# Kernel tuning notes

Hardware: AMD Instinct MI355X
Metric: run time of the kernel (lower is better)

## Reference

```python
import jax, jax.numpy as jnp
import numpy as np

H, D, K = 8, 512, 64
EPS = 1e-12


def _l2norm(x):
    # F.normalize(p=2, dim=-1): x / max(||x||_2, eps)
    n = jnp.sqrt(jnp.sum(x * x, axis=-1, keepdims=True))
    return x / jnp.maximum(n, EPS)


def setup_inputs() -> dict:
    key = jax.random.key(0)
    ks = jax.random.split(key, 8)
    S, B = 1024, 16
    scale = 1.0 / np.sqrt(D)
    return {
        "query": jax.random.normal(ks[0], (S, B, D), dtype=jnp.float32),
        "key": jax.random.normal(ks[1], (S, B, D), dtype=jnp.float32),
        "value": jax.random.normal(ks[2], (S, B, D), dtype=jnp.float32),
        # stacked per-head projection weights, torch Linear convention [out,in]
        "WQ": jax.random.uniform(ks[3], (H, K, D), jnp.float32, -scale, scale),
        "WK": jax.random.uniform(ks[4], (H, K, D), jnp.float32, -scale, scale),
        "WV": jax.random.uniform(ks[5], (H, K, D), jnp.float32, -scale, scale),
        "Wout": jax.random.uniform(ks[6], (D, H * K), jnp.float32,
                                   -1.0 / np.sqrt(H * K), 1.0 / np.sqrt(H * K)),
    }


def reference(query, key, value, WQ, WK, WV, Wout):
    temp = K ** 0.5
    # project all heads at once: [S,B,D] x [H,K,D] -> [B,H,S,K]
    wq = _l2norm(jnp.einsum("sbd,hkd->bhsk", query, WQ))
    wk = _l2norm(jnp.einsum("sbd,hkd->bhsk", key, WK))
    wv = _l2norm(jnp.einsum("sbd,hkd->bhsk", value, WV))
    # cosine-similarity attention scores [B,H,Sq,Sk]
    scores = jnp.einsum("bhsk,bhtk->bhst", wq, wk) / temp
    aff = jax.nn.softmax(scores, axis=-1)
    out = jnp.einsum("bhst,bhtk->bhsk", aff, wv)  # [B,H,S,K]
    # concat heads -> [S,B,H*K] (matches torch per-head concat on last dim)
    Sq, B = query.shape[0], query.shape[1]
    concat = out.transpose(2, 0, 1, 3).reshape(Sq, B, H * K)
    return concat @ Wout.T  # [S,B,D]
```

## Files before the change

kernel.cpp:

```cpp
#include <hip/hip_runtime.h>
#include <cstdint>
#include <cstddef>

typedef unsigned int u32;
typedef unsigned short u16;
typedef __attribute__((ext_vector_type(8))) short short8;
typedef __attribute__((ext_vector_type(4))) float f32x4;

#define S_LEN 1024
#define BATCH 16
#define NHEAD 8
#define DMODEL 512
#define KHD 64
#define NROW (S_LEN * BATCH)

__device__ __forceinline__ u16 f2bf(float f) {
    u32 u = __float_as_uint(f);
    return (u16)((u + 0x7fffu + ((u >> 16) & 1u)) >> 16);
}

__device__ __forceinline__ void gl_lds16(const void* g, void* l) {
    __builtin_amdgcn_global_load_lds(
        (const __attribute__((address_space(1))) void*)(uintptr_t)g,
        (__attribute__((address_space(3))) void*)(uintptr_t)l, 16, 0, 0);
}

__global__ __launch_bounds__(256) void wcvt_kernel(
    const float* __restrict__ WQ, const float* __restrict__ WK,
    const float* __restrict__ WV, const float* __restrict__ Wo,
    u16* __restrict__ dst)
{
    const int m = blockIdx.y;
    const float* __restrict__ src = (m == 0) ? WQ : (m == 1) ? WK : (m == 2) ? WV : Wo;
    const int idx = (blockIdx.x * 256 + threadIdx.x) * 4;
    const float4 v = *(const float4*)(src + idx);
    u16 r[4];
    r[0] = f2bf(v.x); r[1] = f2bf(v.y); r[2] = f2bf(v.z); r[3] = f2bf(v.w);
    *(uint2*)(dst + (size_t)m * DMODEL * DMODEL + idx) = *(uint2*)r;
}

template<int M>
__global__ __launch_bounds__(256) void gemm_kernel(
    const float* __restrict__ A0,
    const float* __restrict__ A1,
    const u16* __restrict__ Abf,
    const u16* __restrict__ Wb,
    u16* __restrict__ outN,
    float* __restrict__ outP)
{
    __shared__ __align__(16) u16 Alds[128 * 64];
    __shared__ __align__(16) u16 Blds[128 * 64];

    const int tid  = threadIdx.x;
    const int wave = tid >> 6;
    const int lane = tid & 63;
    const int m16  = lane & 15;
    const int quad = lane >> 4;
    const int wm   = wave >> 1;
    const int wn   = wave & 1;
    const int n0   = blockIdx.y * 128;
    const int row0 = blockIdx.x * 128;
    const int z    = (M == 1) ? blockIdx.z : 0;
    const int bb   = (M == 2) ? blockIdx.z : 0;

    const float* __restrict__ A32 =
        (M == 1) ? (z ? A1 : A0) : (M == 2) ? (A0 + (size_t)bb * DMODEL) : nullptr;
    const size_t astr = (M == 2) ? (size_t)BATCH * DMODEL : (size_t)DMODEL;
    const u16* __restrict__ B = Wb + ((M == 1) ? (size_t)z * DMODEL * DMODEL : 0);

    f32x4 acc[4][4] = {};

    const int brow   = lane >> 3;
    const int bchunk = (lane & 7) ^ brow;

    for (int kt = 0; kt < DMODEL; kt += 64) {
        __syncthreads();
        {
            u16* la = &Alds[(wave * 32) * 64];
            u16* lb = &Blds[(wave * 32) * 64];
            const u16* bp = B + (size_t)(n0 + wave * 32 + brow) * DMODEL + kt + bchunk * 8;
            if (M == 0) {
                const int colc = kt + bchunk * 8;
                const int hh   = colc >> 6;
                const int kk   = colc & 63;
#pragma unroll
                for (int j = 0; j < 4; j++) {
                    const int i  = row0 + wave * 32 + brow + j * 8;
                    const int ss = i >> 4, bx = i & 15;
                    gl_lds16(Abf + (((size_t)(bx * NHEAD + hh) * S_LEN + ss) * KHD + kk),
                             la + j * 8 * 64);
                    gl_lds16(bp + (size_t)j * 8 * DMODEL, lb + j * 8 * 64);
                }
            } else {
                const int acf = lane & 7;
                float4 av[8];
#pragma unroll
                for (int j = 0; j < 8; j++) {
                    const int rl = wave * 32 + (j & 3) * 8 + brow;
                    const int cf = (j >> 2) * 8 + acf;
                    av[j] = *(const float4*)(A32 + (size_t)(row0 + rl) * astr + kt + cf * 4);
                }
#pragma unroll
                for (int j = 0; j < 4; j++)
                    gl_lds16(bp + (size_t)j * 8 * DMODEL, lb + j * 8 * 64);
#pragma unroll
                for (int j = 0; j < 8; j++) {
                    const int rl = wave * 32 + (j & 3) * 8 + brow;
                    const int cf = (j >> 2) * 8 + acf;
                    u32 lo, hi;
                    asm("v_cvt_pk_bf16_f32 %0, %1, %2" : "=v"(lo) : "v"(av[j].x), "v"(av[j].y));
                    asm("v_cvt_pk_bf16_f32 %0, %1, %2" : "=v"(hi) : "v"(av[j].z), "v"(av[j].w));
                    uint2 pk; pk.x = lo; pk.y = hi;
                    *(uint2*)&Alds[rl * 64 + (((cf >> 1) ^ (rl & 7)) << 3) + ((cf & 1) << 2)] = pk;
                }
            }
        }
        __syncthreads();

#pragma unroll
        for (int half = 0; half < 2; half++) {
            short8 af[4], bfr[4];
#pragma unroll
            for (int mt = 0; mt < 4; mt++)
                af[mt] = *(const short8*)&Alds[(wm * 64 + mt * 16 + m16) * 64 +
                                               (((half << 2) + quad) ^ (m16 & 7)) * 8];
#pragma unroll
            for (int nt = 0; nt < 4; nt++)
                bfr[nt] = *(const short8*)&Blds[(wn * 64 + nt * 16 + m16) * 64 +
                                                (((half << 2) + quad) ^ (m16 & 7)) * 8];
#pragma unroll
            for (int mt = 0; mt < 4; mt++)
#pragma unroll
                for (int nt = 0; nt < 4; nt++)
                    acc[mt][nt] = __builtin_amdgcn_mfma_f32_16x16x32_bf16(af[mt], bfr[nt], acc[mt][nt], 0, 0, 0);
        }
    }

    if (M == 1) {
        const int h = (n0 >> 6) + wn;
        u16* outZ = outN + (size_t)z * BATCH * NHEAD * S_LEN * KHD;
#pragma unroll
        for (int mt = 0; mt < 4; mt++) {
#pragma unroll
            for (int r = 0; r < 4; r++) {
                float ss = 0.0f;
#pragma unroll
                for (int nt = 0; nt < 4; nt++) ss += acc[mt][nt][r] * acc[mt][nt][r];
                ss += __shfl_xor(ss, 1);
                ss += __shfl_xor(ss, 2);
                ss += __shfl_xor(ss, 4);
                ss += __shfl_xor(ss, 8);
                const float sc = 1.0f / fmaxf(sqrtf(ss), 1e-12f);
                const int i = row0 + wm * 64 + mt * 16 + quad * 4 + r;
                const int s = i >> 4, b = i & 15;
                u16* op = outZ + (((size_t)b * NHEAD + h) * S_LEN + s) * KHD;
#pragma unroll
                for (int nt = 0; nt < 4; nt++)
                    op[nt * 16 + m16] = f2bf(acc[mt][nt][r] * sc);
            }
        }
    } else if (M == 2) {
        const int h = (n0 >> 6) + wn;
#pragma unroll
        for (int mt = 0; mt < 4; mt++) {
            float scl[4];
#pragma unroll
            for (int r = 0; r < 4; r++) {
                float ss = 0.0f;
#pragma unroll
                for (int nt = 0; nt < 4; nt++) ss += acc[mt][nt][r] * acc[mt][nt][r];
                ss += __shfl_xor(ss, 1);
                ss += __shfl_xor(ss, 2);
                ss += __shfl_xor(ss, 4);
                ss += __shfl_xor(ss, 8);
                scl[r] = 1.0f / fmaxf(sqrtf(ss), 1e-12f);
            }
            const int sbase = row0 + wm * 64 + mt * 16 + quad * 4;
#pragma unroll
            for (int nt = 0; nt < 4; nt++) {
                const int vcol = nt * 16 + m16;
                uint2 pk;
                pk.x = (u32)f2bf(acc[mt][nt][0] * scl[0]) |
                       ((u32)f2bf(acc[mt][nt][1] * scl[1]) << 16);
                pk.y = (u32)f2bf(acc[mt][nt][2] * scl[2]) |
                       ((u32)f2bf(acc[mt][nt][3] * scl[3]) << 16);
                u16* dp = outN + (((size_t)bb * NHEAD + h) * KHD + vcol) * S_LEN + sbase;
                *(uint2*)dp = pk;
            }
        }
    } else {
#pragma unroll
        for (int mt = 0; mt < 4; mt++) {
#pragma unroll
            for (int r = 0; r < 4; r++) {
                const int i = row0 + wm * 64 + mt * 16 + quad * 4 + r;
                float* op = outP + (size_t)i * DMODEL + n0 + wn * 64;
#pragma unroll
                for (int nt = 0; nt < 4; nt++)
                    op[nt * 16 + m16] = acc[mt][nt][r];
            }
        }
    }
}

__global__ __launch_bounds__(256, 2) void attn_kernel(
    const u16* __restrict__ wq, const u16* __restrict__ wk, const u16* __restrict__ wvT,
    u16* __restrict__ Xout)
{
    __shared__ __align__(16) u16 Klds[2][64 * 64];
    __shared__ __align__(16) u16 Vlds[2][64 * 64];
    __shared__ __align__(16) u16 Plds[4][4][16 * 32];

    const int tid  = threadIdx.x;
    const int wave = tid >> 6;
    const int lane = tid & 63;
    const int m16  = lane & 15;
    const int quad = lane >> 4;
    const int bh   = blockIdx.x;
    const int qt   = blockIdx.y;

    const u16* Qb = wq  + (size_t)bh * S_LEN * KHD;
    const u16* Kb = wk  + (size_t)bh * S_LEN * KHD;
    const u16* Vb = wvT + (size_t)bh * KHD * S_LEN;

    const int qr0 = qt * 256 + wave * 64;
    short8 qf[4][2];
#pragma unroll
    for (int qb = 0; qb < 4; qb++) {
        qf[qb][0] = *(const short8*)(Qb + (size_t)(qr0 + qb * 16 + m16) * KHD + quad * 8);
        qf[qb][1] = *(const short8*)(Qb + (size_t)(qr0 + qb * 16 + m16) * KHD + 32 + quad * 8);
    }

    short8 ones;
#pragma unroll
    for (int j = 0; j < 8; j++) ones[j] = (short)0x3F80;

    f32x4 o[4][4] = {};
    f32x4 ls[4]   = {};
    const float C1 = 0.125f, C2 = 0.0078125f;

    const int srow   = lane >> 3;
    const int schunk = (lane & 7) ^ srow;
    const int r0     = wave * 8 + srow;
    const int pswz   = (m16 >> 1) & 3;

    gl_lds16(Kb + (size_t)r0 * KHD + schunk * 8,               &Klds[0][(wave * 8) * 64]);
    gl_lds16(Kb + (size_t)(r0 + 32) * KHD + schunk * 8,        &Klds[0][(wave * 8 + 32) * 64]);
    gl_lds16(Vb + (size_t)r0 * S_LEN + schunk * 8,             &Vlds[0][(wave * 8) * 64]);
    gl_lds16(Vb + (size_t)(r0 + 32) * S_LEN + schunk * 8,      &Vlds[0][(wave * 8 + 32) * 64]);
    __syncthreads();

    for (int it = 0; it < S_LEN / 64; it++) {
        const int cur = it & 1;

        if (it + 1 < S_LEN / 64) {
            const int nxt = cur ^ 1;
            const int kt0 = (it + 1) * 64;
            gl_lds16(Kb + (size_t)(kt0 + r0) * KHD + schunk * 8,        &Klds[nxt][(wave * 8) * 64]);
            gl_lds16(Kb + (size_t)(kt0 + r0 + 32) * KHD + schunk * 8,   &Klds[nxt][(wave * 8 + 32) * 64]);
            gl_lds16(Vb + (size_t)r0 * S_LEN + kt0 + schunk * 8,        &Vlds[nxt][(wave * 8) * 64]);
            gl_lds16(Vb + (size_t)(r0 + 32) * S_LEN + kt0 + schunk * 8, &Vlds[nxt][(wave * 8 + 32) * 64]);
        }

#pragma unroll
        for (int cc = 0; cc < 2; cc++) {
#pragma unroll
            for (int mm = 0; mm < 2; mm++) {
                const int mt = cc * 2 + mm;
                const short8 kf0 = *(const short8*)&Klds[cur][(mt * 16 + m16) * 64 + (quad ^ (m16 & 7)) * 8];
                const short8 kf1 = *(const short8*)&Klds[cur][(mt * 16 + m16) * 64 + ((4 + quad) ^ (m16 & 7)) * 8];
#pragma unroll
                for (int qb = 0; qb < 4; qb++) {
                    f32x4 s = {};
                    s = __builtin_amdgcn_mfma_f32_16x16x32_bf16(kf0, qf[qb][0], s, 0, 0, 0);
                    s = __builtin_amdgcn_mfma_f32_16x16x32_bf16(kf1, qf[qb][1], s, 0, 0, 0);
                    u32 up[4];
#pragma unroll
                    for (int r = 0; r < 4; r++) {
                        const float y = s[r];
                        const float p = fmaf(fmaf(C2, y, C1), y, 1.0f);
                        up[r] = __float_as_uint(p);
                    }
                    uint2 pk;
                    pk.x = __builtin_amdgcn_perm(up[1], up[0], 0x07060302u);
                    pk.y = __builtin_amdgcn_perm(up[3], up[2], 0x07060302u);
                    *(uint2*)((char*)&Plds[wave][qb][0] + m16 * 64 +
                              ((((mm << 1) + (quad >> 1)) ^ pswz) << 4) + ((quad & 1) << 3)) = pk;
                }
            }

            short8 vfr[4];
#pragma unroll
            for (int vt = 0; vt < 4; vt++)
                vfr[vt] = *(const short8*)&Vlds[cur][(vt * 16 + m16) * 64 +
                                                     (((cc << 2) + quad) ^ (m16 & 7)) * 8];
            __builtin_amdgcn_s_setprio(1);
#pragma unroll
            for (int qb = 0; qb < 4; qb++) {
                const short8 pb = *(const short8*)((const char*)&Plds[wave][qb][0] + m16 * 64 +
                                                   ((quad ^ pswz) << 4));
                ls[qb] = __builtin_amdgcn_mfma_f32_16x16x32_bf16(ones, pb, ls[qb], 0, 0, 0);
#pragma unroll
                for (int vt = 0; vt < 4; vt++)
                    o[qb][vt] = __builtin_amdgcn_mfma_f32_16x16x32_bf16(vfr[vt], pb, o[qb][vt], 0, 0, 0);
            }
            __builtin_amdgcn_s_setprio(0);
        }

        __syncthreads();
    }

    u16* outB = Xout + (size_t)bh * S_LEN * KHD;
#pragma unroll
    for (int qb = 0; qb < 4; qb++) {
        const float inv = 1.0f / ls[qb][0];
        const int qrow = qr0 + qb * 16 + m16;
        u16* cp = outB + (size_t)qrow * KHD;
#pragma unroll
        for (int vt = 0; vt < 4; vt++) {
            uint2 pk;
            pk.x = (u32)f2bf(o[qb][vt][0] * inv) | ((u32)f2bf(o[qb][vt][1] * inv) << 16);
            pk.y = (u32)f2bf(o[qb][vt][2] * inv) | ((u32)f2bf(o[qb][vt][3] * inv) << 16);
            *(uint2*)(cp + vt * 16 + quad * 4) = pk;
        }
    }
}

extern "C" void kernel_launch(void* const* d_in, const int* in_sizes, int n_in,
                              void* d_out, int out_size, void* d_ws, size_t ws_size,
                              hipStream_t stream) {
    const float* q    = (const float*)d_in[0];
    const float* k    = (const float*)d_in[1];
    const float* v    = (const float*)d_in[2];
    const float* WQ   = (const float*)d_in[3];
    const float* WK   = (const float*)d_in[4];
    const float* WV   = (const float*)d_in[5];
    const float* Wout = (const float*)d_in[6];
    float* out = (float*)d_out;

    const size_t per = (size_t)BATCH * NHEAD * S_LEN * KHD;
    u16* wsQKV = (u16*)d_ws;
    u16* wsW   = wsQKV + 3 * per;

    wcvt_kernel<<<dim3(256, 4), 256, 0, stream>>>(WQ, WK, WV, Wout, wsW);

    gemm_kernel<1><<<dim3(NROW / 128, DMODEL / 128, 2), 256, 0, stream>>>(
        q, k, nullptr, wsW, wsQKV, nullptr);

    gemm_kernel<2><<<dim3(S_LEN / 128, DMODEL / 128, BATCH), 256, 0, stream>>>(
        v, nullptr, nullptr, wsW + (size_t)2 * DMODEL * DMODEL, wsQKV + 2 * per, nullptr);

    attn_kernel<<<dim3(BATCH * NHEAD, S_LEN / 256), 256, 0, stream>>>(
        wsQKV, wsQKV + per, wsQKV + 2 * per, wsQKV);

    gemm_kernel<0><<<dim3(NROW / 128, DMODEL / 128, 1), 256, 0, stream>>>(
        nullptr, nullptr, wsQKV, wsW + (size_t)3 * DMODEL * DMODEL, nullptr, out);
}
```

Measured before the change: 239.6 us.

## Double-buffer GEMM LDS tiles to overlap next-tile loads with MFMA compute

The GEMM main loop now uses two LDS buffers for A and B. Loads for tile k+1 (async global-to-LDS for B and bf16 A, register loads for fp32 A) are issued before computing tile k, and the fp32 A tile is converted and written to LDS after compute. This replaces the two barriers per iteration with one and aims to hide global-memory latency behind the matrix math. In exchange it doubles LDS use to 64 KB per block and holds the prefetched A registers live across compute. The launch bounds now request 2 blocks per CU, which may cap registers.

```diff
diff --git a/kernel.cpp b/kernel.cpp
--- a/kernel.cpp
+++ b/kernel.cpp
@@ -40,7 +40,7 @@
 }
 
 template<int M>
-__global__ __launch_bounds__(256) void gemm_kernel(
+__global__ __launch_bounds__(256, 2) void gemm_kernel(
     const float* __restrict__ A0,
     const float* __restrict__ A1,
     const u16* __restrict__ Abf,
@@ -48,8 +48,8 @@
     u16* __restrict__ outN,
     float* __restrict__ outP)
 {
-    __shared__ __align__(16) u16 Alds[128 * 64];
-    __shared__ __align__(16) u16 Blds[128 * 64];
+    __shared__ __align__(16) u16 Alds[2][128 * 64];
+    __shared__ __align__(16) u16 Blds[2][128 * 64];
 
     const int tid  = threadIdx.x;
     const int wave = tid >> 6;
@@ -72,68 +72,85 @@
 
     const int brow   = lane >> 3;
     const int bchunk = (lane & 7) ^ brow;
-
-    for (int kt = 0; kt < DMODEL; kt += 64) {
-        __syncthreads();
-        {
-            u16* la = &Alds[(wave * 32) * 64];
-            u16* lb = &Blds[(wave * 32) * 64];
-            const u16* bp = B + (size_t)(n0 + wave * 32 + brow) * DMODEL + kt + bchunk * 8;
-            if (M == 0) {
-                const int colc = kt + bchunk * 8;
-                const int hh   = colc >> 6;
-                const int kk   = colc & 63;
-#pragma unroll
-                for (int j = 0; j < 4; j++) {
-                    const int i  = row0 + wave * 32 + brow + j * 8;
-                    const int ss = i >> 4, bx = i & 15;
-                    gl_lds16(Abf + (((size_t)(bx * NHEAD + hh) * S_LEN + ss) * KHD + kk),
-                             la + j * 8 * 64);
-                    gl_lds16(bp + (size_t)j * 8 * DMODEL, lb + j * 8 * 64);
-                }
-            } else {
-                const int acf = lane & 7;
-                float4 av[8];
-#pragma unroll
-                for (int j = 0; j < 8; j++) {
-                    const int rl = wave * 32 + (j & 3) * 8 + brow;
-                    const int cf = (j >> 2) * 8 + acf;
-                    av[j] = *(const float4*)(A32 + (size_t)(row0 + rl) * astr + kt + cf * 4);
-                }
-#pragma unroll
-                for (int j = 0; j < 4; j++)
-                    gl_lds16(bp + (size_t)j * 8 * DMODEL, lb + j * 8 * 64);
-#pragma unroll
-                for (int j = 0; j < 8; j++) {
-                    const int rl = wave * 32 + (j & 3) * 8 + brow;
-                    const int cf = (j >> 2) * 8 + acf;
-                    u32 lo, hi;
-                    asm("v_cvt_pk_bf16_f32 %0, %1, %2" : "=v"(lo) : "v"(av[j].x), "v"(av[j].y));
-                    asm("v_cvt_pk_bf16_f32 %0, %1, %2" : "=v"(hi) : "v"(av[j].z), "v"(av[j].w));
-                    uint2 pk; pk.x = lo; pk.y = hi;
-                    *(uint2*)&Alds[rl * 64 + (((cf >> 1) ^ (rl & 7)) << 3) + ((cf & 1) << 2)] = pk;
-                }
-            }
-        }
-        __syncthreads();
-
+    const int acf    = lane & 7;
+
+    float4 av[8];
+
+    auto stage_B = [&](int kt, int b) {
+        const u16* bp = B + (size_t)(n0 + wave * 32 + brow) * DMODEL + kt + bchunk * 8;
+        u16* lb = &Blds[b][(wave * 32) * 64];
+#pragma unroll
+        for (int j = 0; j < 4; j++)
+            gl_lds16(bp + (size_t)j * 8 * DMODEL, lb + j * 8 * 64);
+    };
+    auto stage_A0 = [&](int kt, int b) {
+        u16* la = &Alds[b][(wave * 32) * 64];
+        const int colc = kt + bchunk * 8;
+        const int hh   = colc >> 6;
+        const int kk   = colc & 63;
+#pragma unroll
+        for (int j = 0; j < 4; j++) {
+            const int i  = row0 + wave * 32 + brow + j * 8;
+            const int ss = i >> 4, bx = i & 15;
+            gl_lds16(Abf + (((size_t)(bx * NHEAD + hh) * S_LEN + ss) * KHD + kk),
+                     la + j * 8 * 64);
+        }
+    };
+    auto load_A = [&](int kt) {
+#pragma unroll
+        for (int j = 0; j < 8; j++) {
+            const int rl = wave * 32 + (j & 3) * 8 + brow;
+            const int cf = (j >> 2) * 8 + acf;
+            av[j] = *(const float4*)(A32 + (size_t)(row0 + rl) * astr + kt + cf * 4);
+        }
+    };
+    auto write_A = [&](int b) {
+#pragma unroll
+        for (int j = 0; j < 8; j++) {
+            const int rl = wave * 32 + (j & 3) * 8 + brow;
+            const int cf = (j >> 2) * 8 + acf;
+            u32 lo, hi;
+            asm("v_cvt_pk_bf16_f32 %0, %1, %2" : "=v"(lo) : "v"(av[j].x), "v"(av[j].y));
+            asm("v_cvt_pk_bf16_f32 %0, %1, %2" : "=v"(hi) : "v"(av[j].z), "v"(av[j].w));
+            uint2 pk; pk.x = lo; pk.y = hi;
+            *(uint2*)&Alds[b][rl * 64 + (((cf >> 1) ^ (rl & 7)) << 3) + ((cf & 1) << 2)] = pk;
+        }
+    };
+    auto compute = [&](int b) {
 #pragma unroll
         for (int half = 0; half < 2; half++) {
             short8 af[4], bfr[4];
 #pragma unroll
             for (int mt = 0; mt < 4; mt++)
-                af[mt] = *(const short8*)&Alds[(wm * 64 + mt * 16 + m16) * 64 +
-                                               (((half << 2) + quad) ^ (m16 & 7)) * 8];
+                af[mt] = *(const short8*)&Alds[b][(wm * 64 + mt * 16 + m16) * 64 +
+                                                  (((half << 2) + quad) ^ (m16 & 7)) * 8];
 #pragma unroll
             for (int nt = 0; nt < 4; nt++)
-                bfr[nt] = *(const short8*)&Blds[(wn * 64 + nt * 16 + m16) * 64 +
-                                                (((half << 2) + quad) ^ (m16 & 7)) * 8];
+                bfr[nt] = *(const short8*)&Blds[b][(wn * 64 + nt * 16 + m16) * 64 +
+                                                   (((half << 2) + quad) ^ (m16 & 7)) * 8];
 #pragma unroll
             for (int mt = 0; mt < 4; mt++)
 #pragma unroll
                 for (int nt = 0; nt < 4; nt++)
                     acc[mt][nt] = __builtin_amdgcn_mfma_f32_16x16x32_bf16(af[mt], bfr[nt], acc[mt][nt], 0, 0, 0);
         }
+    };
+
+    if (M == 0) { stage_A0(0, 0); stage_B(0, 0); }
+    else        { load_A(0); stage_B(0, 0); write_A(0); }
+    __syncthreads();
+
+#pragma unroll 2
+    for (int it = 0; it < 8; it++) {
+        const int cur = it & 1;
+        const int nxt = cur ^ 1;
+        if (it < 7) {
+            if (M == 0) { stage_A0((it + 1) * 64, nxt); stage_B((it + 1) * 64, nxt); }
+            else        { load_A((it + 1) * 64);        stage_B((it + 1) * 64, nxt); }
+        }
+        compute(cur);
+        if (M != 0 && it < 7) write_A(nxt);
+        __syncthreads();
     }
 
     if (M == 1) {
```

New measurement: 241.7 us. No clear change (+0.9%).

## Split output projection into double-buffered 512-thread GEMM kernel

Applied to the files above, without the earlier changes.

The output-projection GEMM (M==0 path) moves out of the templated gemm_kernel into a dedicated gemm_out_kernel. It uses 8 waves per block, each holding a 32x64 accumulator tile, and double-buffered LDS with async global-to-LDS loads. Explicit vmcnt waits and barriers let the next K-tile load overlap the current tile's MFMA work. This aims to hide memory latency and raise occupancy, at the cost of twice the LDS per block and hand-tuned wait counts that must match the issued loads.

```diff
diff --git a/kernel.cpp b/kernel.cpp
--- a/kernel.cpp
+++ b/kernel.cpp
@@ -43,10 +43,8 @@
 __global__ __launch_bounds__(256) void gemm_kernel(
     const float* __restrict__ A0,
     const float* __restrict__ A1,
-    const u16* __restrict__ Abf,
     const u16* __restrict__ Wb,
-    u16* __restrict__ outN,
-    float* __restrict__ outP)
+    u16* __restrict__ outN)
 {
     __shared__ __align__(16) u16 Alds[128 * 64];
     __shared__ __align__(16) u16 Blds[128 * 64];
@@ -64,7 +62,7 @@
     const int bb   = (M == 2) ? blockIdx.z : 0;
 
     const float* __restrict__ A32 =
-        (M == 1) ? (z ? A1 : A0) : (M == 2) ? (A0 + (size_t)bb * DMODEL) : nullptr;
+        (M == 1) ? (z ? A1 : A0) : (A0 + (size_t)bb * DMODEL);
     const size_t astr = (M == 2) ? (size_t)BATCH * DMODEL : (size_t)DMODEL;
     const u16* __restrict__ B = Wb + ((M == 1) ? (size_t)z * DMODEL * DMODEL : 0);
 
@@ -72,47 +70,32 @@
 
     const int brow   = lane >> 3;
     const int bchunk = (lane & 7) ^ brow;
+    const int acf    = lane & 7;
 
     for (int kt = 0; kt < DMODEL; kt += 64) {
         __syncthreads();
         {
-            u16* la = &Alds[(wave * 32) * 64];
+            const u16* bp = B + (size_t)(n0 + wave * 32 + brow) * DMODEL + kt + bchunk * 8;
             u16* lb = &Blds[(wave * 32) * 64];
-            const u16* bp = B + (size_t)(n0 + wave * 32 + brow) * DMODEL + kt + bchunk * 8;
-            if (M == 0) {
-                const int colc = kt + bchunk * 8;
-                const int hh   = colc >> 6;
-                const int kk   = colc & 63;
-#pragma unroll
-                for (int j = 0; j < 4; j++) {
-                    const int i  = row0 + wave * 32 + brow + j * 8;
-                    const int ss = i >> 4, bx = i & 15;
-                    gl_lds16(Abf + (((size_t)(bx * NHEAD + hh) * S_LEN + ss) * KHD + kk),
-                             la + j * 8 * 64);
-                    gl_lds16(bp + (size_t)j * 8 * DMODEL, lb + j * 8 * 64);
-                }
-            } else {
-                const int acf = lane & 7;
-                float4 av[8];
-#pragma unroll
-                for (int j = 0; j < 8; j++) {
-                    const int rl = wave * 32 + (j & 3) * 8 + brow;
-                    const int cf = (j >> 2) * 8 + acf;
-                    av[j] = *(const float4*)(A32 + (size_t)(row0 + rl) * astr + kt + cf * 4);
-                }
-#pragma unroll
-                for (int j = 0; j < 4; j++)
-                    gl_lds16(bp + (size_t)j * 8 * DMODEL, lb + j * 8 * 64);
-#pragma unroll
-                for (int j = 0; j < 8; j++) {
-                    const int rl = wave * 32 + (j & 3) * 8 + brow;
-                    const int cf = (j >> 2) * 8 + acf;
-                    u32 lo, hi;
-                    asm("v_cvt_pk_bf16_f32 %0, %1, %2" : "=v"(lo) : "v"(av[j].x), "v"(av[j].y));
-                    asm("v_cvt_pk_bf16_f32 %0, %1, %2" : "=v"(hi) : "v"(av[j].z), "v"(av[j].w));
-                    uint2 pk; pk.x = lo; pk.y = hi;
-                    *(uint2*)&Alds[rl * 64 + (((cf >> 1) ^ (rl & 7)) << 3) + ((cf & 1) << 2)] = pk;
-                }
+            float4 av[8];
+#pragma unroll
+            for (int j = 0; j < 8; j++) {
+                const int rl = wave * 32 + (j & 3) * 8 + brow;
+                const int cf = (j >> 2) * 8 + acf;
+                av[j] = *(const float4*)(A32 + (size_t)(row0 + rl) * astr + kt + cf * 4);
+            }
+#pragma unroll
+            for (int j = 0; j < 4; j++)
+                gl_lds16(bp + (size_t)j * 8 * DMODEL, lb + j * 8 * 64);
+#pragma unroll
+            for (int j = 0; j < 8; j++) {
+                const int rl = wave * 32 + (j & 3) * 8 + brow;
+                const int cf = (j >> 2) * 8 + acf;
+                u32 lo, hi;
+                asm("v_cvt_pk_bf16_f32 %0, %1, %2" : "=v"(lo) : "v"(av[j].x), "v"(av[j].y));
+                asm("v_cvt_pk_bf16_f32 %0, %1, %2" : "=v"(hi) : "v"(av[j].z), "v"(av[j].w));
+                uint2 pk; pk.x = lo; pk.y = hi;
+                *(uint2*)&Alds[rl * 64 + (((cf >> 1) ^ (rl & 7)) << 3) + ((cf & 1) << 2)] = pk;
             }
         }
         __syncthreads();
@@ -153,13 +136,15 @@
                 const float sc = 1.0f / fmaxf(sqrtf(ss), 1e-12f);
                 const int i = row0 + wm * 64 + mt * 16 + quad * 4 + r;
                 const int s = i >> 4, b = i & 15;
-                u16* op = outZ + (((size_t)b * NHEAD + h) * S_LEN + s) * KHD;
+                u16* op = outN + (size_t)z * BATCH * NHEAD * S_LEN * KHD +
+                          (((size_t)b * NHEAD + h) * S_LEN + s) * KHD;
+                (void)outZ;
 #pragma unroll
                 for (int nt = 0; nt < 4; nt++)
                     op[nt * 16 + m16] = f2bf(acc[mt][nt][r] * sc);
             }
         }
-    } else if (M == 2) {
+    } else {
         const int h = (n0 >> 6) + wn;
 #pragma unroll
         for (int mt = 0; mt < 4; mt++) {
@@ -188,17 +173,101 @@
                 *(uint2*)dp = pk;
             }
         }
-    } else {
-#pragma unroll
-        for (int mt = 0; mt < 4; mt++) {
-#pragma unroll
-            for (int r = 0; r < 4; r++) {
-                const int i = row0 + wm * 64 + mt * 16 + quad * 4 + r;
-                float* op = outP + (size_t)i * DMODEL + n0 + wn * 64;
+    }
+}
+
+__global__ __launch_bounds__(512, 2) void gemm_out_kernel(
+    const u16* __restrict__ Abf,
+    const u16* __restrict__ Wb,
+    float* __restrict__ outP)
+{
+    __shared__ __align__(16) u16 Alds[2][128 * 64];
+    __shared__ __align__(16) u16 Blds[2][128 * 64];
+
+    const int tid  = threadIdx.x;
+    const int wave = tid >> 6;
+    const int lane = tid & 63;
+    const int m16  = lane & 15;
+    const int quad = lane >> 4;
+    const int wm   = wave >> 1;
+    const int wn   = wave & 1;
+    const int n0   = blockIdx.y * 128;
+    const int row0 = blockIdx.x * 128;
+
+    const int brow   = lane >> 3;
+    const int bchunk = (lane & 7) ^ brow;
+
+    f32x4 acc[2][4] = {};
+
+    auto stage = [&](int kt, int b) {
+        const int colc = kt + bchunk * 8;
+        const int hh   = colc >> 6;
+        const int kk   = colc & 63;
+        u16* la = &Alds[b][(wave * 16) * 64];
+#pragma unroll
+        for (int j = 0; j < 2; j++) {
+            const int i  = row0 + wave * 16 + j * 8 + brow;
+            const int ss = i >> 4, bx = i & 15;
+            gl_lds16(Abf + (((size_t)(bx * NHEAD + hh) * S_LEN + ss) * KHD + kk),
+                     la + j * 8 * 64);
+        }
+        const u16* bp = Wb + (size_t)(n0 + wave * 16 + brow) * DMODEL + kt + bchunk * 8;
+        u16* lb = &Blds[b][(wave * 16) * 64];
+#pragma unroll
+        for (int j = 0; j < 2; j++)
+            gl_lds16(bp + (size_t)j * 8 * DMODEL, lb + j * 8 * 64);
+    };
+    auto compute = [&](int b) {
+#pragma unroll
+        for (int half = 0; half < 2; half++) {
+            short8 af[2], bfr[4];
+#pragma unroll
+            for (int mt = 0; mt < 2; mt++)
+                af[mt] = *(const short8*)&Alds[b][(wm * 32 + mt * 16 + m16) * 64 +
+                                                  (((half << 2) + quad) ^ (m16 & 7)) * 8];
+#pragma unroll
+            for (int nt = 0; nt < 4; nt++)
+                bfr[nt] = *(const short8*)&Blds[b][(wn * 64 + nt * 16 + m16) * 64 +
+                                                   (((half << 2) + quad) ^ (m16 & 7)) * 8];
+#pragma unroll
+            for (int mt = 0; mt < 2; mt++)
 #pragma unroll
                 for (int nt = 0; nt < 4; nt++)
-                    op[nt * 16 + m16] = acc[mt][nt][r];
-            }
+                    acc[mt][nt] = __builtin_amdgcn_mfma_f32_16x16x32_bf16(af[mt], bfr[nt], acc[mt][nt], 0, 0, 0);
+        }
+    };
+
+    stage(0, 0);
+    stage(64, 1);
+    asm volatile("s_waitcnt vmcnt(4)" ::: "memory");
+    __builtin_amdgcn_s_barrier();
+    __builtin_amdgcn_sched_barrier(0);
+
+#pragma unroll
+    for (int t = 0; t < 8; t++) {
+        compute(t & 1);
+        if (t < 6) {
+            __builtin_amdgcn_s_barrier();
+            __builtin_amdgcn_sched_barrier(0);
+            stage((t + 2) * 64, t & 1);
+        }
+        if (t < 7) {
+            if (t < 6) asm volatile("s_waitcnt vmcnt(4)" ::: "memory");
+            else       asm volatile("s_waitcnt vmcnt(0)" ::: "memory");
+            __builtin_amdgcn_s_barrier();
+            __builtin_amdgcn_sched_barrier(0);
+        }
+    }
+
+#pragma unroll
+    for (int mt = 0; mt < 2; mt++) {
+#pragma unroll
+        for (int r = 0; r < 4; r++) {
+            const int i = row0 + wm * 32 + mt * 16 + quad * 4 + r;
+            float* op = outP + (size_t)i * DMODEL + n0 + wn * 64;
+#pragma unroll
+            for (int nt = 0; nt < 4; nt++)
+                op[nt * 16 + m16] = acc[mt][nt][r];
         }
     }
 }
@@ -345,14 +414,14 @@
     wcvt_kernel<<<dim3(256, 4), 256, 0, stream>>>(WQ, WK, WV, Wout, wsW);
 
     gemm_kernel<1><<<dim3(NROW / 128, DMODEL / 128, 2), 256, 0, stream>>>(
-        q, k, nullptr, wsW, wsQKV, nullptr);
+        q, k, wsW, wsQKV);
 
     gemm_kernel<2><<<dim3(S_LEN / 128, DMODEL / 128, BATCH), 256, 0, stream>>>(
-        v, nullptr, nullptr, wsW + (size_t)2 * DMODEL * DMODEL, wsQKV + 2 * per, nullptr);
+        v, nullptr, wsW + (size_t)2 * DMODEL * DMODEL, wsQKV + 2 * per);
 
     attn_kernel<<<dim3(BATCH * NHEAD, S_LEN / 256), 256, 0, stream>>>(
         wsQKV, wsQKV + per, wsQKV + 2 * per, wsQKV);
 
-    gemm_kernel<0><<<dim3(NROW / 128, DMODEL / 128, 1), 256, 0, stream>>>(
-        nullptr, nullptr, wsQKV, wsW + (size_t)3 * DMODEL * DMODEL, nullptr, out);
-}
+    gemm_out_kernel<<<dim3(NROW / 128, DMODEL / 128), 512, 0, stream>>>(
+        wsQKV, wsW + (size_t)3 * DMODEL * DMODEL, out);
+}
```

Result: no change. 238.9 us (-0.3%).
